# Performance work log

Hardware: AMD Instinct MI355X
Metric: run time of the kernel (lower is better)

The kernel has to match this reference:

```python
import jax, jax.numpy as jnp
import numpy as np

D_MODEL = 1024
N_HEADS = 16
D_HEAD = D_MODEL // N_HEADS
B, T = 2, 2048


def setup_inputs() -> dict:
    key = jax.random.key(0)
    ks = jax.random.split(key, 8)
    s = 1.0 / np.sqrt(D_MODEL)
    return {
        "x": jax.random.normal(ks[0], (B, T, D_MODEL), dtype=jnp.float32),
        "ln_g": jnp.ones((D_MODEL,), jnp.float32),
        "ln_b": jnp.zeros((D_MODEL,), jnp.float32),
        "w_qkv": jax.random.normal(ks[1], (D_MODEL, 3 * D_MODEL), jnp.float32) * s,
        "b_qkv": jnp.zeros((3 * D_MODEL,), jnp.float32),
        "w_gate": jax.random.normal(ks[2], (D_MODEL, D_MODEL), jnp.float32) * s,
        "b_gate": jnp.zeros((D_MODEL,), jnp.float32),
        "w_proj": jax.random.normal(ks[3], (D_MODEL, D_MODEL), jnp.float32) * s,
        "b_proj": jnp.zeros((D_MODEL,), jnp.float32),
    }


def reference(x, ln_g, ln_b, w_qkv, b_qkv, w_gate, b_gate, w_proj, b_proj):
    Bb, Tt, Dd = x.shape
    H, dh = N_HEADS, D_HEAD

    # LayerNorm (eps=1e-5, torch default)
    mu = jnp.mean(x, axis=-1, keepdims=True)
    var = jnp.mean((x - mu) ** 2, axis=-1, keepdims=True)
    x_norm = (x - mu) / jnp.sqrt(var + 1e-5) * ln_g + ln_b

    qkv = x_norm @ w_qkv + b_qkv
    q, k, v = jnp.split(qkv, 3, axis=-1)

    # concept gate on the RAW input x (not x_norm), normalized by its mean
    gate_sig = jax.nn.sigmoid(x @ w_gate + b_gate)
    gate_norm = gate_sig / (jnp.mean(gate_sig, axis=-1, keepdims=True) + 1e-5)
    q = q * gate_norm
    k = k * gate_norm

    # [B,T,D] -> [B,H,T,dh]
    def to_heads(t):
        return t.reshape(Bb, Tt, H, dh).transpose(0, 2, 1, 3)

    q, k, v = to_heads(q), to_heads(k), to_heads(v)

    q = jax.nn.elu(q) + 1.0
    k = jax.nn.elu(k) + 1.0

    # materialized outer-product cumsum (faithful to source formulation)
    kv = jnp.einsum("bhtd,bhtm->bhtdm", k, v)          # [B,H,T,dh,dh]
    kv_cumsum = jnp.cumsum(kv, axis=2)
    out_num = jnp.einsum("bhtd,bhtdm->bhtm", q, kv_cumsum)
    k_cumsum = jnp.cumsum(k, axis=2)
    out_den = jnp.einsum("bhtd,bhtd->bht", q, k_cumsum)[..., None] + 1e-5
    out = out_num / out_den                              # [B,H,T,dh]

    out = out.transpose(0, 2, 1, 3).reshape(Bb, Tt, Dd)
    return out @ w_proj + b_proj
```

## Files before the change

### kernel.cpp

```cpp
#include <hip/hip_runtime.h>
#include <math.h>

constexpr int D      = 1024;
constexpr int H      = 16;
constexpr int DH     = 64;
constexpr int Bb     = 2;
constexpr int T      = 2048;
constexpr int BT     = Bb * T;
constexpr int CHUNK  = 64;
constexpr int NC     = T / CHUNK;
constexpr int LS     = 72;

typedef __attribute__((ext_vector_type(8))) short bf16x8;
typedef __attribute__((ext_vector_type(4))) float f32x4;

#define GLOAD_LDS16(gp, lp) \
    __builtin_amdgcn_global_load_lds((const __attribute__((address_space(1))) void*)(gp), \
                                     (__attribute__((address_space(3))) void*)(lp), 16, 0, 0)

__device__ __forceinline__ short to_bf16(float f) {
    unsigned u = __float_as_uint(f);
    unsigned r = (u + 0x7fffu + ((u >> 16) & 1u)) >> 16;
    return (short)r;
}
__device__ __forceinline__ float bf2f(short s) {
    return __uint_as_float(((unsigned)(unsigned short)s) << 16);
}

__device__ __forceinline__ float elu1(float x) {
    return x > 0.0f ? x + 1.0f : __expf(x);
}


__global__ __launch_bounds__(256) void pre_kernel(const float* __restrict__ x,
                                                  const float* __restrict__ g,
                                                  const float* __restrict__ b,
                                                  const float* __restrict__ wq,
                                                  const float* __restrict__ wg,
                                                  const float* __restrict__ wp,
                                                  short* __restrict__ ynb,
                                                  short* __restrict__ xbb,
                                                  short* __restrict__ wTcomb,
                                                  short* __restrict__ wTp,
                                                  float* __restrict__ gmean) {
    __shared__ short tile2[64 * 72];
    int bid = blockIdx.x;
    int tid = threadIdx.x;
    if (bid < 1024) {
        int row  = bid * 4 + (tid >> 6);
        int lane = tid & 63;
        const float* xr = x + (size_t)row * D;
        float4 xv[4];
        float s = 0.0f;
        #pragma unroll
        for (int i = 0; i < 4; ++i) {
            xv[i] = *(const float4*)(xr + i * 256 + lane * 4);
            s += xv[i].x + xv[i].y + xv[i].z + xv[i].w;
        }
        #pragma unroll
        for (int off = 32; off > 0; off >>= 1) s += __shfl_xor(s, off, 64);
        float mu = s * (1.0f / D);
        float vs = 0.0f;
        #pragma unroll
        for (int i = 0; i < 4; ++i) {
            float d0 = xv[i].x - mu, d1 = xv[i].y - mu;
            float d2 = xv[i].z - mu, d3 = xv[i].w - mu;
            vs += d0 * d0 + d1 * d1 + d2 * d2 + d3 * d3;
        }
        #pragma unroll
        for (int off = 32; off > 0; off >>= 1) vs += __shfl_xor(vs, off, 64);
        float rstd = rsqrtf(vs * (1.0f / D) + 1e-5f);
        if (lane == 0) gmean[row] = 0.0f;
        #pragma unroll
        for (int i = 0; i < 4; ++i) {
            int cc = i * 256 + lane * 4;
            float4 gv = *(const float4*)(g + cc);
            float4 bv = *(const float4*)(b + cc);
            short4 o, xo;
            o.x = to_bf16((xv[i].x - mu) * rstd * gv.x + bv.x);
            o.y = to_bf16((xv[i].y - mu) * rstd * gv.y + bv.y);
            o.z = to_bf16((xv[i].z - mu) * rstd * gv.z + bv.z);
            o.w = to_bf16((xv[i].w - mu) * rstd * gv.w + bv.w);
            xo.x = to_bf16(xv[i].x); xo.y = to_bf16(xv[i].y);
            xo.z = to_bf16(xv[i].z); xo.w = to_bf16(xv[i].w);
            *(short4*)(ynb + (size_t)row * D + cc) = o;
            *(short4*)(xbb + (size_t)row * D + cc) = xo;
        }
    } else {
        int t2 = bid - 1024;
        const float* W; short* Wt; int N; int t;
        if (t2 < 768)       { W = wq; Wt = wTcomb;                       N = 3072; t = t2; }
        else if (t2 < 1024) { W = wg; Wt = wTcomb + (size_t)3072 * 1024; N = 1024; t = t2 - 768; }
        else                { W = wp; Wt = wTp;                          N = 1024; t = t2 - 1024; }
        int ntn = N >> 6;
        int nb = (t % ntn) * 64, kb = (t / ntn) * 64;

        int k  = tid >> 2;
        int n4 = (tid & 3) * 16;
        const float* src = W + (size_t)(kb + k) * N + nb + n4;
        float4 f0 = *(const float4*)(src);
        float4 f1 = *(const float4*)(src + 4);
        float4 f2 = *(const float4*)(src + 8);
        float4 f3 = *(const float4*)(src + 12);
        bf16x8 h0, h1;
        h0[0] = to_bf16(f0.x); h0[1] = to_bf16(f0.y); h0[2] = to_bf16(f0.z); h0[3] = to_bf16(f0.w);
        h0[4] = to_bf16(f1.x); h0[5] = to_bf16(f1.y); h0[6] = to_bf16(f1.z); h0[7] = to_bf16(f1.w);
        h1[0] = to_bf16(f2.x); h1[1] = to_bf16(f2.y); h1[2] = to_bf16(f2.z); h1[3] = to_bf16(f2.w);
        h1[4] = to_bf16(f3.x); h1[5] = to_bf16(f3.y); h1[6] = to_bf16(f3.z); h1[7] = to_bf16(f3.w);
        *(bf16x8*)&tile2[k * 72 + n4]     = h0;
        *(bf16x8*)&tile2[k * 72 + n4 + 8] = h1;
        __syncthreads();

        int n   = tid >> 2;
        int k16 = (tid & 3) * 16;
        bf16x8 o0, o1;
        #pragma unroll
        for (int j = 0; j < 8; ++j) o0[j] = tile2[(k16 + j) * 72 + n];
        #pragma unroll
        for (int j = 0; j < 8; ++j) o1[j] = tile2[(k16 + 8 + j) * 72 + n];
        short* dst = Wt + (size_t)(nb + n) * 1024 + kb + k16;
        *(bf16x8*)dst       = o0;
        *(bf16x8*)(dst + 8) = o1;
    }
}

#define SWZ(os) ((os) ^ ((((os) >> 6) & 3) << 3))
#define BARX() __builtin_amdgcn_s_barrier()
#define LGKM0() asm volatile("s_waitcnt lgkmcnt(0)" ::: "memory")
#define VMW(n) asm volatile("s_waitcnt vmcnt(" #n ")" ::: "memory")
#define MEMFENCE() asm volatile("" ::: "memory")

#define STG(Mp, rb, t, kc, isB) do {                                                       \
    short* _b = ldsbuf + ((((t) & 1)) << 15) + (((((isB) << 1) | (kc))) << 13) + wid * 1024; \
    const short* _g = (Mp) + (size_t)((rb) + wid * 32 + s_r) * 1024 + (t) * 64 + (kc) * 32 + s_c; \
    GLOAD_LDS16(_g, _b);                                                                   \
    GLOAD_LDS16(_g + (size_t)16 * 1024, _b + 512);                                         \
} while (0)

#define FRAGA(t, kc, mi) (*(const bf16x8*)(ldsbuf + (((t) & 1) << 15) + ((kc) << 13) + \
    SWZ((wm * 128 + (mi) * 16 + fr) * 32 + fk)))
#define FRAGB(t, kc, ni) (*(const bf16x8*)(ldsbuf + (((t) & 1) << 15) + ((2 + (kc)) << 13) + \
    SWZ((wn * 64 + (ni) * 16 + fr) * 32 + fk)))

#define GROUP(t, S1, S2, S3, S4, W2, W4) do {                                              \
    bf16x8 af[8], bq[4];                                                                   \
    _Pragma("unroll") for (int mi = 0; mi < 8; ++mi) af[mi] = FRAGA(t, 0, mi);             \
    bq[0] = FRAGB(t, 0, 0); bq[1] = FRAGB(t, 0, 1);                                        \
    if (S1) STG(Wt, col0, (t) + 1, 1, 1);                                                  \
    BARX(); LGKM0();                                                                       \
    __builtin_amdgcn_s_setprio(1);                                                         \
    _Pragma("unroll") for (int mi = 0; mi < 8; ++mi) {                                     \
        acc[mi][0] = __builtin_amdgcn_mfma_f32_16x16x32_bf16(af[mi], bq[0], acc[mi][0], 0, 0, 0); \
        acc[mi][1] = __builtin_amdgcn_mfma_f32_16x16x32_bf16(af[mi], bq[1], acc[mi][1], 0, 0, 0); \
    }                                                                                      \
    __builtin_amdgcn_s_setprio(0);                                                         \
    BARX();                                                                                \
    bq[2] = FRAGB(t, 0, 2); bq[3] = FRAGB(t, 0, 3);                                        \
    if (S2) STG(Ap, row0, (t) + 2, 0, 0);                                                  \
    BARX(); LGKM0();                                                                       \
    __builtin_amdgcn_s_setprio(1);                                                         \
    _Pragma("unroll") for (int mi = 0; mi < 8; ++mi) {                                     \
        acc[mi][2] = __builtin_amdgcn_mfma_f32_16x16x32_bf16(af[mi], bq[2], acc[mi][2], 0, 0, 0); \
        acc[mi][3] = __builtin_amdgcn_mfma_f32_16x16x32_bf16(af[mi], bq[3], acc[mi][3], 0, 0, 0); \
    }                                                                                      \
    __builtin_amdgcn_s_setprio(0);                                                         \
    W2; BARX();                                                                            \
    _Pragma("unroll") for (int mi = 0; mi < 8; ++mi) af[mi] = FRAGA(t, 1, mi);             \
    bq[0] = FRAGB(t, 1, 0); bq[1] = FRAGB(t, 1, 1);                                        \
    if (S3) STG(Wt, col0, (t) + 2, 0, 1);                                                  \
    BARX(); LGKM0();                                                                       \
    __builtin_amdgcn_s_setprio(1);                                                         \
    _Pragma("unroll") for (int mi = 0; mi < 8; ++mi) {                                     \
        acc[mi][0] = __builtin_amdgcn_mfma_f32_16x16x32_bf16(af[mi], bq[0], acc[mi][0], 0, 0, 0); \
        acc[mi][1] = __builtin_amdgcn_mfma_f32_16x16x32_bf16(af[mi], bq[1], acc[mi][1], 0, 0, 0); \
    }                                                                                      \
    __builtin_amdgcn_s_setprio(0);                                                         \
    BARX();                                                                                \
    bq[2] = FRAGB(t, 1, 2); bq[3] = FRAGB(t, 1, 3);                                        \
    if (S4) STG(Ap, row0, (t) + 2, 1, 0);                                                  \
    BARX(); LGKM0();                                                                       \
    __builtin_amdgcn_s_setprio(1);                                                         \
    _Pragma("unroll") for (int mi = 0; mi < 8; ++mi) {                                     \
        acc[mi][2] = __builtin_amdgcn_mfma_f32_16x16x32_bf16(af[mi], bq[2], acc[mi][2], 0, 0, 0); \
        acc[mi][3] = __builtin_amdgcn_mfma_f32_16x16x32_bf16(af[mi], bq[3], acc[mi][3], 0, 0, 0); \
    }                                                                                      \
    __builtin_amdgcn_s_setprio(0);                                                         \
    W4; BARX();                                                                            \
} while (0)

__global__ __launch_bounds__(512, 2) void gemm_fused_qkvgate(const short* __restrict__ xnb,
                                                             const short* __restrict__ xb,
                                                             const short* __restrict__ Wt,
                                                             const float* __restrict__ b_qkv,
                                                             const float* __restrict__ b_gate,
                                                             short* __restrict__ qkvb,
                                                             short* __restrict__ sigb,
                                                             float* __restrict__ gmean) {
    __shared__ short ldsbuf[2 * 32768];

    const int bid   = blockIdx.x;
    const int xcd   = bid & 7;
    const int local = bid >> 3;
    const int cx = xcd & 3, ry = xcd >> 2;
    const int bxx = cx * 4 + (local & 3);
    const int byy = ry * 8 + (local >> 2);
    const int row0 = byy * 256;
    const int col0 = bxx * 256;
    const bool isg = (col0 >= 3 * D);
    const short* Ap = isg ? xb : xnb;

    const int tid  = threadIdx.x;
    const int wid  = tid >> 6;
    const int lane = tid & 63;
    const int wm = wid >> 2;
    const int wn = wid & 3;
    const int fr = lane & 15;
    const int fk = (lane >> 4) * 8;

    const int s_r = lane >> 2;
    const int s_c = 8 * ((lane & 3) ^ ((lane >> 3) & 3));

    f32x4 acc[8][4] = {};

    STG(Ap, row0, 0, 0, 0); MEMFENCE();
    STG(Wt, col0, 0, 0, 1); MEMFENCE();
    STG(Ap, row0, 0, 1, 0); MEMFENCE();
    STG(Wt, col0, 0, 1, 1); MEMFENCE();
    STG(Ap, row0, 1, 0, 0); MEMFENCE();
    STG(Wt, col0, 1, 0, 1); MEMFENCE();
    STG(Ap, row0, 1, 1, 0);
    VMW(10);
    BARX();

    for (int t = 0; t < 14; ++t) GROUP(t, 1, 1, 1, 1, VMW(10), VMW(10));
    GROUP(14, 1, 0, 0, 0, VMW(8), VMW(4));
    GROUP(15, 0, 0, 0, 0, VMW(0), (void)0);

    const int ccol  = lane & 15;
    const int crow4 = (lane >> 4) * 4;
    if (!isg) {
        #pragma unroll
        for (int mi = 0; mi < 8; ++mi) {
            #pragma unroll
            for (int ni = 0; ni < 4; ++ni) {
                int col = col0 + wn * 64 + ni * 16 + ccol;
                float bv = b_qkv[col];
                #pragma unroll
                for (int r = 0; r < 4; ++r) {
                    int row = row0 + wm * 128 + mi * 16 + crow4 + r;
                    qkvb[(size_t)row * (3 * D) + col] = to_bf16(acc[mi][ni][r] + bv);
                }
            }
        }
    } else {
        #pragma unroll
        for (int mi = 0; mi < 8; ++mi) {
            #pragma unroll
            for (int r = 0; r < 4; ++r) {
                int lrow = row0 + wm * 128 + mi * 16 + crow4 + r;
                float psum = 0.0f;
                #pragma unroll
                for (int ni = 0; ni < 4; ++ni) {
                    int col = col0 + wn * 64 + ni * 16 + ccol - 3 * D;
                    float v = acc[mi][ni][r] + b_gate[col];
                    float sv = 1.0f / (1.0f + __expf(-v));
                    sigb[(size_t)lrow * D + col] = to_bf16(sv);
                    psum += sv;
                }
                psum += __shfl_xor(psum, 1, 64);
                psum += __shfl_xor(psum, 2, 64);
                psum += __shfl_xor(psum, 4, 64);
                psum += __shfl_xor(psum, 8, 64);
                if (ccol == 0) atomicAdd(&gmean[lrow], psum);
            }
        }
    }
}

__global__ __launch_bounds__(256) void chunk_state_mfma(const short* __restrict__ qkvb,
                                                        const short* __restrict__ sigb,
                                                        const float* __restrict__ gmean,
                                                        float* __restrict__ Sc,
                                                        float* __restrict__ zc) {
    __shared__ short Kt[DH * LS];
    __shared__ short Vt[DH * LS];
    int idx = blockIdx.x;
    int c = idx & (NC - 1), h = (idx >> 5) & (H - 1), b = idx >> 9;
    size_t bt0 = (size_t)b * T + c * CHUNK;
    const short* kbase = qkvb + bt0 * (3 * D) + D + h * DH;
    const short* vbase = kbase + D;
    const short* sbase = sigb + bt0 * D + h * DH;
    int tid = threadIdx.x;

    #pragma unroll
    for (int l = 0; l < 2; ++l) {
        int i  = tid + l * 256;
        int t  = i >> 3;
        int d8 = (i & 7) * 8;
        float invm = 1.0f / (gmean[bt0 + t] * (1.0f / D) + 1e-5f);
        bf16x8 kv = *(const bf16x8*)(kbase + (size_t)t * (3 * D) + d8);
        bf16x8 vv = *(const bf16x8*)(vbase + (size_t)t * (3 * D) + d8);
        bf16x8 sg = *(const bf16x8*)(sbase + (size_t)t * D + d8);
        #pragma unroll
        for (int j = 0; j < 8; ++j) {
            float gn = bf2f(sg[j]) * invm;
            Kt[(d8 + j) * LS + t] = to_bf16(elu1(bf2f(kv[j]) * gn));
            Vt[(d8 + j) * LS + t] = vv[j];
        }
    }
    __syncthreads();

    const int wv = tid >> 6, lane = tid & 63;
    const int fr = lane & 15, quad = lane >> 4;
    const int fk = quad * 8, crow4 = quad * 4, ccol = lane & 15;
    const int mbase = wv * 16;

    bf16x8 af0 = *(const bf16x8*)&Vt[(mbase + fr) * LS + fk];
    bf16x8 af1 = *(const bf16x8*)&Vt[(mbase + fr) * LS + 32 + fk];

    f32x4 acc[4] = {};
    #pragma unroll
    for (int n = 0; n < 4; ++n) {
        bf16x8 bk0 = *(const bf16x8*)&Kt[(n * 16 + fr) * LS + fk];
        bf16x8 bk1 = *(const bf16x8*)&Kt[(n * 16 + fr) * LS + 32 + fk];
        acc[n] = __builtin_amdgcn_mfma_f32_16x16x32_bf16(af0, bk0, acc[n], 0, 0, 0);
        acc[n] = __builtin_amdgcn_mfma_f32_16x16x32_bf16(af1, bk1, acc[n], 0, 0, 0);
    }

    float* Sd = Sc + (size_t)idx * (DH * DH);
    #pragma unroll
    for (int n = 0; n < 4; ++n)
        #pragma unroll
        for (int r = 0; r < 4; ++r)
            Sd[(mbase + crow4 + r) * DH + n * 16 + ccol] = acc[n][r];

    {
        int d = tid >> 2, p = tid & 3;
        bf16x8 k0 = *(const bf16x8*)&Kt[d * LS + p * 16];
        bf16x8 k1 = *(const bf16x8*)&Kt[d * LS + p * 16 + 8];
        float zs = 0.0f;
        #pragma unroll
        for (int j = 0; j < 8; ++j) zs += bf2f(k0[j]) + bf2f(k1[j]);
        zs += __shfl_xor(zs, 1, 64);
        zs += __shfl_xor(zs, 2, 64);
        if (p == 0) zc[(size_t)idx * DH + d] = zs;
    }
}

__global__ __launch_bounds__(256) void chunk_prefix_kernel(const float* __restrict__ S,
                                                           short* __restrict__ Spb,
                                                           float* __restrict__ z) {
    int bh   = blockIdx.x >> 4;
    int part = blockIdx.x & 15;
    int e    = part * 256 + threadIdx.x;
    const float* Sb = S + (size_t)bh * NC * DH * DH;
    short* Pb = Spb + (size_t)bh * NC * DH * DH;
    float v[NC];
    #pragma unroll
    for (int c = 0; c < NC; ++c) v[c] = Sb[(size_t)c * DH * DH + e];
    float acc = 0.0f;
    #pragma unroll
    for (int c = 0; c < NC; ++c) {
        Pb[(size_t)c * DH * DH + e] = to_bf16(acc);
        acc += v[c];
    }
    if (part == 0 && threadIdx.x < DH) {
        float* zb = z + (size_t)bh * NC * DH + threadIdx.x;
        float zv[NC];
        #pragma unroll
        for (int c = 0; c < NC; ++c) zv[c] = zb[(size_t)c * DH];
        float za = 0.0f;
        #pragma unroll
        for (int c = 0; c < NC; ++c) {
            zb[(size_t)c * DH] = za;
            za += zv[c];
        }
    }
}

__global__ __launch_bounds__(256) void chunk_attn_mfma(const short* __restrict__ qkvb,
                                                       const short* __restrict__ sigb,
                                                       const float* __restrict__ gmean,
                                                       const short* __restrict__ Spb,
                                                       const float* __restrict__ zc,
                                                       short* __restrict__ attnb) {
    __shared__ short Qs[CHUNK * LS];
    __shared__ short Ks[CHUNK * LS];
    __shared__ short Vt[DH * LS];
    __shared__ short Ss[DH * LS];
    __shared__ float zpL[DH];
    __shared__ float den[CHUNK];
    short* As = Ks;

    int idx = blockIdx.x;
    int c = idx & (NC - 1), h = (idx >> 5) & (H - 1), b = idx >> 9;
    size_t bt0 = (size_t)b * T + c * CHUNK;
    const short* qbase = qkvb + bt0 * (3 * D) + h * DH;
    const short* kbase = qbase + D;
    const short* vbase = qbase + 2 * D;
    const short* sbase = sigb + bt0 * D + h * DH;
    const short* spb = Spb + (size_t)idx * (DH * DH);
    int tid = threadIdx.x;

    #pragma unroll
    for (int l = 0; l < 2; ++l) {
        int i  = tid + l * 256;
        int t  = i >> 3;
        int d8 = (i & 7) * 8;
        float invm = 1.0f / (gmean[bt0 + t] * (1.0f / D) + 1e-5f);
        bf16x8 qv = *(const bf16x8*)(qbase + (size_t)t * (3 * D) + d8);
        bf16x8 kv = *(const bf16x8*)(kbase + (size_t)t * (3 * D) + d8);
        bf16x8 vv = *(const bf16x8*)(vbase + (size_t)t * (3 * D) + d8);
        bf16x8 sg = *(const bf16x8*)(sbase + (size_t)t * D + d8);
        bf16x8 qg, kg;
        #pragma unroll
        for (int j = 0; j < 8; ++j) {
            float gn = bf2f(sg[j]) * invm;
            qg[j] = to_bf16(elu1(bf2f(qv[j]) * gn));
            kg[j] = to_bf16(elu1(bf2f(kv[j]) * gn));
            Vt[(d8 + j) * LS + t] = vv[j];
        }
        *(bf16x8*)&Qs[t * LS + d8] = qg;
        *(bf16x8*)&Ks[t * LS + d8] = kg;
        *(bf16x8*)&Ss[t * LS + d8] = *(const bf16x8*)(spb + (size_t)i * 8);
    }
    if (tid < DH) zpL[tid] = zc[(size_t)idx * DH + tid];
    __syncthreads();

    const int wv = tid >> 6, lane = tid & 63;
    const int fr = lane & 15, quad = lane >> 4;
    const int fk = quad * 8, crow4 = quad * 4, ccol = lane & 15;
    const int tbase = wv * 16;

    bf16x8 aq0 = *(const bf16x8*)&Qs[(tbase + fr) * LS + fk];
    bf16x8 aq1 = *(const bf16x8*)&Qs[(tbase + fr) * LS + 32 + fk];

    f32x4 accs[4] = {};
    #pragma unroll
    for (int n = 0; n < 4; ++n) {
        bf16x8 bk0 = *(const bf16x8*)&Ks[(n * 16 + fr) * LS + fk];
        bf16x8 bk1 = *(const bf16x8*)&Ks[(n * 16 + fr) * LS + 32 + fk];
        accs[n] = __builtin_amdgcn_mfma_f32_16x16x32_bf16(aq0, bk0, accs[n], 0, 0, 0);
        accs[n] = __builtin_amdgcn_mfma_f32_16x16x32_bf16(aq1, bk1, accs[n], 0, 0, 0);
    }
    __syncthreads();

    float part[4] = {0.f, 0.f, 0.f, 0.f};
    #pragma unroll
    for (int n = 0; n < 4; ++n) {
        #pragma unroll
        for (int r = 0; r < 4; ++r) {
            int tt = tbase + crow4 + r;
            int ss = n * 16 + ccol;
            float v = (ss <= tt) ? accs[n][r] : 0.0f;
            part[r] += v;
            As[tt * LS + ss] = to_bf16(v);
        }
    }
    #pragma unroll
    for (int r = 0; r < 4; ++r) {
        part[r] += __shfl_xor(part[r], 1, 64);
        part[r] += __shfl_xor(part[r], 2, 64);
        part[r] += __shfl_xor(part[r], 4, 64);
        part[r] += __shfl_xor(part[r], 8, 64);
    }
    if (fr == 0) {
        #pragma unroll
        for (int r = 0; r < 4; ++r) den[tbase + crow4 + r] = part[r];
    }
    __syncthreads();

    {
        int t = tid >> 2, p = tid & 3;
        bf16x8 q0 = *(const bf16x8*)&Qs[t * LS + p * 16];
        bf16x8 q1 = *(const bf16x8*)&Qs[t * LS + p * 16 + 8];
        float qz = 0.0f;
        #pragma unroll
        for (int j = 0; j < 8; ++j)
            qz += bf2f(q0[j]) * zpL[p * 16 + j] + bf2f(q1[j]) * zpL[p * 16 + 8 + j];
        qz += __shfl_xor(qz, 1, 64);
        qz += __shfl_xor(qz, 2, 64);
        if (p == 0) den[t] += qz + 1e-5f;
    }

    f32x4 acco[4] = {};
    #pragma unroll
    for (int m4 = 0; m4 < 4; ++m4) {
        bf16x8 bs0 = *(const bf16x8*)&Ss[(m4 * 16 + fr) * LS + fk];
        bf16x8 bs1 = *(const bf16x8*)&Ss[(m4 * 16 + fr) * LS + 32 + fk];
        acco[m4] = __builtin_amdgcn_mfma_f32_16x16x32_bf16(aq0, bs0, acco[m4], 0, 0, 0);
        acco[m4] = __builtin_amdgcn_mfma_f32_16x16x32_bf16(aq1, bs1, acco[m4], 0, 0, 0);
    }
    bf16x8 aa0 = *(const bf16x8*)&As[(tbase + fr) * LS + fk];
    bf16x8 aa1 = *(const bf16x8*)&As[(tbase + fr) * LS + 32 + fk];
    #pragma unroll
    for (int m4 = 0; m4 < 4; ++m4) {
        bf16x8 bv0 = *(const bf16x8*)&Vt[(m4 * 16 + fr) * LS + fk];
        bf16x8 bv1 = *(const bf16x8*)&Vt[(m4 * 16 + fr) * LS + 32 + fk];
        acco[m4] = __builtin_amdgcn_mfma_f32_16x16x32_bf16(aa0, bv0, acco[m4], 0, 0, 0);
        acco[m4] = __builtin_amdgcn_mfma_f32_16x16x32_bf16(aa1, bv1, acco[m4], 0, 0, 0);
    }
    __syncthreads();

    short* obase = attnb + bt0 * D + h * DH;
    #pragma unroll
    for (int r = 0; r < 4; ++r) {
        int tt = tbase + crow4 + r;
        float rv = 1.0f / den[tt];
        #pragma unroll
        for (int m4 = 0; m4 < 4; ++m4)
            obase[(size_t)tt * D + m4 * 16 + ccol] = to_bf16(acco[m4][r] * rv);
    }
}

#define SWZ64(os) ((os) ^ ((((os) >> 6) & 7) << 3))

__global__ __launch_bounds__(256) void gemm_proj64(const short* __restrict__ A,
                                                   const short* __restrict__ Bt,
                                                   const float* __restrict__ bias,
                                                   float* __restrict__ C) {
    constexpr int BK = 64, K = 1024;
    constexpr int N = 1024;
    __shared__ short Als[64 * BK];
    __shared__ short Bls[128 * BK];

    const int bid   = blockIdx.x;
    const int xcd   = bid & 7;
    const int local = bid >> 3;
    const int cx = xcd & 3, ry = xcd >> 2;
    const int lx = local & 1, ly = local >> 1;
    const int bxx = cx * 2 + lx;
    const int byy = ry * 32 + ly;

    const int tid  = threadIdx.x;
    const int wave = tid >> 6;
    const int lane = tid & 63;
    const int row0 = byy * 64;
    const int col0 = bxx * 128;
    const int wn = wave * 32;

    f32x4 acc[4][2] = {};
    const int fr = lane & 15;
    const int fk = (lane >> 4) * 8;

    for (int k0 = 0; k0 < K; k0 += BK) {
        __syncthreads();
        #pragma unroll
        for (int u = 0; u < 2; ++u) {
            int slot = tid + u * 256;
            int r = slot >> 3, c8 = (slot & 7) ^ (r & 7);
            GLOAD_LDS16(A + (size_t)(row0 + r) * K + k0 + c8 * 8, &Als[slot * 8]);
        }
        #pragma unroll
        for (int u = 0; u < 4; ++u) {
            int slot = tid + u * 256;
            int r = slot >> 3, c8 = (slot & 7) ^ (r & 7);
            GLOAD_LDS16(Bt + (size_t)(col0 + r) * K + k0 + c8 * 8, &Bls[slot * 8]);
        }
        __syncthreads();

        #pragma unroll
        for (int ck = 0; ck < 2; ++ck) {
            bf16x8 af[4], bfr[2];
            #pragma unroll
            for (int i = 0; i < 4; ++i)
                af[i] = *(const bf16x8*)&Als[SWZ64((i * 16 + fr) * BK + ck * 32 + fk)];
            #pragma unroll
            for (int j = 0; j < 2; ++j)
                bfr[j] = *(const bf16x8*)&Bls[SWZ64((wn + j * 16 + fr) * BK + ck * 32 + fk)];
            #pragma unroll
            for (int mi = 0; mi < 4; ++mi)
                #pragma unroll
                for (int ni = 0; ni < 2; ++ni)
                    acc[mi][ni] = __builtin_amdgcn_mfma_f32_16x16x32_bf16(af[mi], bfr[ni], acc[mi][ni], 0, 0, 0);
        }
    }

    const int ccol  = lane & 15;
    const int crow4 = (lane >> 4) * 4;
    #pragma unroll
    for (int mi = 0; mi < 4; ++mi) {
        #pragma unroll
        for (int ni = 0; ni < 2; ++ni) {
            int col = col0 + wn + ni * 16 + ccol;
            float bv = bias[col];
            #pragma unroll
            for (int r = 0; r < 4; ++r) {
                int row = row0 + mi * 16 + crow4 + r;
                C[(size_t)row * N + col] = acc[mi][ni][r] + bv;
            }
        }
    }
}

extern "C" void kernel_launch(void* const* d_in, const int* in_sizes, int n_in,
                              void* d_out, int out_size, void* d_ws, size_t ws_size,
                              hipStream_t stream) {
    const float* x      = (const float*)d_in[0];
    const float* ln_g   = (const float*)d_in[1];
    const float* ln_b   = (const float*)d_in[2];
    const float* w_qkv  = (const float*)d_in[3];
    const float* b_qkv  = (const float*)d_in[4];
    const float* w_gate = (const float*)d_in[5];
    const float* b_gate = (const float*)d_in[6];
    const float* w_proj = (const float*)d_in[7];
    const float* b_proj = (const float*)d_in[8];
    float* out = (float*)d_out;

    short* xnb   = (short*)d_ws;
    short* xb    = xnb + (size_t)BT * D;
    short* wTc   = xb + (size_t)BT * D;
    short* wTp   = wTc + (size_t)4096 * 1024;
    short* qkvb  = wTp + (size_t)D * D;
    short* sigb  = qkvb + (size_t)BT * 3 * D;
    short* attnb = sigb + (size_t)BT * D;
    float* zc    = (float*)(attnb + (size_t)BT * D);
    float* gmean = zc + (size_t)Bb * H * NC * DH;
    float* Sc    = (float*)xnb;
    short* Spb   = wTc;

    pre_kernel<<<1024 + 1280, 256, 0, stream>>>(x, ln_g, ln_b, w_qkv, w_gate, w_proj,
                                                xnb, xb, wTc, wTp, gmean);
    gemm_fused_qkvgate<<<256, 512, 0, stream>>>(
        xnb, xb, wTc, b_qkv, b_gate, qkvb, sigb, gmean);
    chunk_state_mfma<<<Bb * H * NC, 256, 0, stream>>>(qkvb, sigb, gmean, Sc, zc);
    chunk_prefix_kernel<<<Bb * H * 16, 256, 0, stream>>>(Sc, Spb, zc);
    chunk_attn_mfma<<<Bb * H * NC, 256, 0, stream>>>(qkvb, sigb, gmean, Spb, zc, attnb);
    gemm_proj64<<<512, 256, 0, stream>>>(attnb, wTp, b_proj, out);
}
```

Before: 186.6 us.

## Fuse chunk prefix scan into chunk_state via last-block atomic counter

```diff
diff --git a/kernel.cpp b/kernel.cpp
--- a/kernel.cpp
+++ b/kernel.cpp
@@ -42,11 +42,13 @@
                                                   short* __restrict__ xbb,
                                                   short* __restrict__ wTcomb,
                                                   short* __restrict__ wTp,
-                                                  float* __restrict__ gmean) {
+                                                  float* __restrict__ gmean,
+                                                  unsigned* __restrict__ done) {
     __shared__ short tile2[64 * 72];
     int bid = blockIdx.x;
     int tid = threadIdx.x;
     if (bid < 1024) {
+        if (bid == 0 && tid < Bb * H) done[tid] = 0;
         int row  = bid * 4 + (tid >> 6);
         int lane = tid & 63;
         const float* xr = x + (size_t)row * D;
@@ -281,9 +283,12 @@
                                                         const short* __restrict__ sigb,
                                                         const float* __restrict__ gmean,
                                                         float* __restrict__ Sc,
-                                                        float* __restrict__ zc) {
+                                                        short* __restrict__ Spb,
+                                                        float* __restrict__ zc,
+                                                        unsigned* __restrict__ done) {
     __shared__ short Kt[DH * LS];
     __shared__ short Vt[DH * LS];
+    __shared__ int isLast;
     int idx = blockIdx.x;
     int c = idx & (NC - 1), h = (idx >> 5) & (H - 1), b = idx >> 9;
     size_t bt0 = (size_t)b * T + c * CHUNK;
@@ -345,35 +350,43 @@
         zs += __shfl_xor(zs, 2, 64);
         if (p == 0) zc[(size_t)idx * DH + d] = zs;
     }
-}
-
-__global__ __launch_bounds__(256) void chunk_prefix_kernel(const float* __restrict__ S,
-                                                           short* __restrict__ Spb,
-                                                           float* __restrict__ z) {
-    int bh   = blockIdx.x >> 4;
-    int part = blockIdx.x & 15;
-    int e    = part * 256 + threadIdx.x;
-    const float* Sb = S + (size_t)bh * NC * DH * DH;
-    short* Pb = Spb + (size_t)bh * NC * DH * DH;
-    float v[NC];
-    #pragma unroll
-    for (int c = 0; c < NC; ++c) v[c] = Sb[(size_t)c * DH * DH + e];
-    float acc = 0.0f;
-    #pragma unroll
-    for (int c = 0; c < NC; ++c) {
-        Pb[(size_t)c * DH * DH + e] = to_bf16(acc);
-        acc += v[c];
-    }
-    if (part == 0 && threadIdx.x < DH) {
-        float* zb = z + (size_t)bh * NC * DH + threadIdx.x;
-        float zv[NC];
-        #pragma unroll
-        for (int c = 0; c < NC; ++c) zv[c] = zb[(size_t)c * DH];
-        float za = 0.0f;
-        #pragma unroll
-        for (int c = 0; c < NC; ++c) {
-            zb[(size_t)c * DH] = za;
-            za += zv[c];
+
+    __threadfence();
+    __syncthreads();
+    if (tid == 0) {
+        unsigned old = __hip_atomic_fetch_add(&done[idx >> 5], 1u,
+                                              __ATOMIC_ACQ_REL, __HIP_MEMORY_SCOPE_AGENT);
+        isLast = (old == NC - 1);
+    }
+    __syncthreads();
+    if (isLast) {
+        int grp = idx >> 5;
+        const float* Sb = Sc + (size_t)grp * NC * DH * DH;
+        short* Pb = Spb + (size_t)grp * NC * DH * DH;
+        #pragma unroll 1
+        for (int pass = 0; pass < 16; ++pass) {
+            int e = pass * 256 + tid;
+            float v[NC];
+            #pragma unroll
+            for (int cc = 0; cc < NC; ++cc) v[cc] = Sb[(size_t)cc * (DH * DH) + e];
+            float a = 0.0f;
+            #pragma unroll
+            for (int cc = 0; cc < NC; ++cc) {
+                Pb[(size_t)cc * (DH * DH) + e] = to_bf16(a);
+                a += v[cc];
+            }
+        }
+        if (tid < DH) {
+            float* zb = zc + (size_t)grp * NC * DH + tid;
+            float zv[NC];
+            #pragma unroll
+            for (int cc = 0; cc < NC; ++cc) zv[cc] = zb[(size_t)cc * DH];
+            float za = 0.0f;
+            #pragma unroll
+            for (int cc = 0; cc < NC; ++cc) {
+                zb[(size_t)cc * DH] = za;
+                za += zv[cc];
+            }
         }
     }
 }
@@ -616,15 +629,15 @@
     short* attnb = sigb + (size_t)BT * D;
     float* zc    = (float*)(attnb + (size_t)BT * D);
     float* gmean = zc + (size_t)Bb * H * NC * DH;
+    unsigned* done = (unsigned*)(gmean + BT);
     float* Sc    = (float*)xnb;
     short* Spb   = wTc;
 
     pre_kernel<<<1024 + 1280, 256, 0, stream>>>(x, ln_g, ln_b, w_qkv, w_gate, w_proj,
-                                                xnb, xb, wTc, wTp, gmean);
+                                                xnb, xb, wTc, wTp, gmean, done);
     gemm_fused_qkvgate<<<256, 512, 0, stream>>>(
         xnb, xb, wTc, b_qkv, b_gate, qkvb, sigb, gmean);
-    chunk_state_mfma<<<Bb * H * NC, 256, 0, stream>>>(qkvb, sigb, gmean, Sc, zc);
-    chunk_prefix_kernel<<<Bb * H * 16, 256, 0, stream>>>(Sc, Spb, zc);
+    chunk_state_mfma<<<Bb * H * NC, 256, 0, stream>>>(qkvb, sigb, gmean, Sc, Spb, zc, done);
     chunk_attn_mfma<<<Bb * H * NC, 256, 0, stream>>>(qkvb, sigb, gmean, Spb, zc, attnb);
     gemm_proj64<<<512, 256, 0, stream>>>(attnb, wTp, b_proj, out);
 }
```

Measured after the change: 358.0 us. +91.9%, slower.
